# Optimization experiments

Measured on AMD Instinct MI355X. Metric: run time of the kernel, lower is better.

## Reference

```python
import jax, jax.numpy as jnp
import numpy as np

# graph/batch constants
B, N_PER, DEG, FEAT, K = 64, 1024, 16, 64, 10
N = B * N_PER            # 65536 total nodes
E = N * DEG              # 1048576 edges
HID = 2 * FEAT           # 128


def setup_inputs() -> dict:
    key = jax.random.key(0)
    ks = jax.random.split(key, 10)
    x = jax.random.normal(ks[0], (N, FEAT), jnp.float32)
    # intra-graph edges: local indices in [0, n) offset by graph id * n
    offs = (jnp.arange(B, dtype=jnp.int32) * N_PER)[:, None]
    edge_src = (jax.random.randint(ks[1], (B, N_PER * DEG), 0, N_PER, jnp.int32) + offs).reshape(-1)
    edge_dst = (jax.random.randint(ks[2], (B, N_PER * DEG), 0, N_PER, jnp.int32) + offs).reshape(-1)
    uniforms = jax.random.uniform(ks[3], (N, 3 * K), jnp.float32, 1e-6, 1.0 - 1e-6)

    def lin(k, i, o):
        s = 1.0 / np.sqrt(i)
        return jax.random.uniform(k, (i, o), jnp.float32, -s, s)

    return {
        "x": x, "edge_src": edge_src, "edge_dst": edge_dst, "uniforms": uniforms,
        "W0": lin(ks[4], FEAT, HID), "b0": jnp.zeros((HID,), jnp.float32),
        "W1": lin(ks[5], HID, HID), "b1": jnp.zeros((HID,), jnp.float32),
        "Wf": lin(ks[6], HID, HID), "bf": jnp.zeros((HID,), jnp.float32),
        "W2": lin(ks[7], 2 * HID, HID), "b2": jnp.zeros((HID,), jnp.float32),
        "W3": lin(ks[8], HID, 1), "b3": jnp.zeros((1,), jnp.float32),
    }


def _gcn_norm(src, dst):
    # GCNConv: add self-loops, symmetric deg^{-1/2} normalization
    loop = jnp.arange(N, dtype=src.dtype)
    s = jnp.concatenate([src, loop])
    d = jnp.concatenate([dst, loop])
    deg = jnp.zeros((N,), jnp.float32).at[d].add(1.0)
    dinv = jax.lax.rsqrt(deg)  # deg >= 1 because of self-loops
    return s, d, dinv[s] * dinv[d]


def _gcn(h, W, b, s, d, norm):
    h = h @ W                                                   # [N, out]
    agg = jnp.zeros((N, W.shape[1]), h.dtype).at[d].add(h[s] * norm[:, None])
    return agg + b


def reference(x, edge_src, edge_dst, uniforms, W0, b0, W1, b1, Wf, bf, W2, b2, W3, b3):
    s, d, norm = _gcn_norm(edge_src, edge_dst)
    # conv0 + global max pool + fc1 -> per-graph global info
    h0 = jax.nn.relu(_gcn(x, W0, b0, s, d, norm))               # [N, HID]
    glob = jnp.max(h0.reshape(B, N_PER, HID), axis=1) @ Wf + bf  # [B, HID]
    # two applications of the SAME conv1 (as in the source)
    h = jax.nn.relu(_gcn(h0, W1, b1, s, d, norm))
    h = jax.nn.relu(_gcn(h, W1, b1, s, d, norm))
    # ConcatenateLayer: [local, tiled global] per node (dropout is eval identity)
    h = jnp.concatenate([h, jnp.repeat(glob, N_PER, axis=0)], axis=-1)  # [N, 2*HID]
    h = jax.nn.relu(_gcn(h, W2, b2, s, d, norm))
    logits = _gcn(h, W3, b3, s, d, norm).reshape(B, N_PER)      # [B, n]
    # SampleConcrete (eval): per-graph top-k threshold mask
    th = jax.lax.top_k(logits, K)[0][:, -1]                     # kth-largest per graph
    mask = (logits >= th[:, None]).astype(jnp.float32)
    return mask.reshape(N, 1)
```

## Files before the change

kernel.cpp:

```cpp
#include <hip/hip_runtime.h>
#include <math.h>

#define NB    64
#define NPER  1024
#define NTOT  65536
#define ETOT  1048576
#define FEAT  64
#define HID   128
#define KSEL  10
#define MAXDEG 64


typedef __attribute__((ext_vector_type(8))) short bf16x8;
typedef __attribute__((ext_vector_type(4))) float f32x4;

#define ASLOT(a, q) (((a) << 2) + ((q) ^ (((a) >> 1) & 3)))
#define GSLOT(p, r) (((p) * 64 + ((r) ^ ((p) & 7))) * 8)

static __device__ __forceinline__ unsigned short f2bf(float x) {
    unsigned u = __float_as_uint(x);
    return (unsigned short)((u + 0x7FFFu + ((u >> 16) & 1u)) >> 16);
}
static __device__ __forceinline__ float bf2f(unsigned short s) {
    return __uint_as_float(((unsigned)s) << 16);
}

__global__ __launch_bounds__(256) void csr_k(const int* __restrict__ src,
                                             const int* __restrict__ dst,
                                             int* __restrict__ cnt,
                                             unsigned short* __restrict__ col16) {
    int e = blockIdx.x * 256 + threadIdx.x;
    if (e >= ETOT) return;
    int d = dst[e];
    int s = src[e];
    int pos = atomicAdd(&cnt[d], 1);
    col16[(size_t)pos * NTOT + d] = (unsigned short)(s & (NPER - 1));
}

__global__ __launch_bounds__(256) void pack_k(const float* __restrict__ W0,
                                              const float* __restrict__ W1,
                                              const float* __restrict__ W2,
                                              unsigned short* __restrict__ Wph,
                                              unsigned short* __restrict__ Wpl,
                                              float* __restrict__ part,
                                              int* __restrict__ cnt) {
    int t = blockIdx.x * 256 + threadIdx.x;
    for (int i = t; i < NTOT; i += 160 * 256) cnt[i] = 0;
    if (blockIdx.x == 0) {
        for (int i = threadIdx.x; i < NB * 128; i += 256) part[i] = 0.f;
    }
    if (t >= 320 * 128) return;
    int k = t >> 7;
    int c = t & 127;
    float v;
    size_t mb;
    int kk;
    if (k < 64)       { kk = k;       v = W0[kk * 128 + c]; mb = 0; }
    else if (k < 192) { kk = k - 64;  v = W1[kk * 128 + c]; mb = (size_t)64 * 128; }
    else              { kk = k - 192; v = W2[kk * 128 + c]; mb = (size_t)192 * 128; }
    unsigned short h  = f2bf(v);
    unsigned short lo = f2bf(v - bf2f(h));
    size_t d = mb + ((size_t)(kk >> 3) * 128 + c) * 8 + (kk & 7);
    Wph[d] = h;
    Wpl[d] = lo;
}

__global__ __launch_bounds__(1024) void agg_k(const float* __restrict__ Z,
                                              const float* __restrict__ x,
                                              const unsigned short* __restrict__ col16,
                                              const int* __restrict__ cnt,
                                              unsigned short* __restrict__ Ah,
                                              unsigned short* __restrict__ Al,
                                              int cshift,
                                              float* __restrict__ fvec,
                                              const float* __restrict__ Wf,
                                              const float* __restrict__ bfv,
                                              const float* __restrict__ W2g,
                                              float* __restrict__ gproj,
                                              const float* __restrict__ part) {
    __shared__ float4 sy4[4096];
    int t = threadIdx.x;

    if (Wf && (int)blockIdx.x >= (int)gridDim.x - NB) {
        float* sm = (float*)sy4;
        float* mp = sm;
        float* ps = sm + 128;
        float* gl = sm + 128 + 1024;
        int gg = blockIdx.x - (gridDim.x - NB);
        int o = t & 127, s8 = t >> 7;
        if (t < 128) mp[t] = part[(size_t)gg * 128 + t];
        __syncthreads();
        float p = 0.f;
#pragma unroll
        for (int q = 0; q < 16; ++q) { int k = s8 * 16 + q; p += mp[k] * Wf[(size_t)k * 128 + o]; }
        ps[t] = p;
        __syncthreads();
        if (t < 128) {
            float a = bfv[t];
#pragma unroll
            for (int q = 0; q < 8; ++q) a += ps[q * 128 + t];
            gl[t] = a;
        }
        __syncthreads();
        p = 0.f;
#pragma unroll
        for (int q = 0; q < 16; ++q) { int k = s8 * 16 + q; p += gl[k] * W2g[(size_t)(128 + k) * 128 + o]; }
        ps[t] = p;
        __syncthreads();
        if (t < 128) {
            float a = 0.f;
#pragma unroll
            for (int q = 0; q < 8; ++q) a += ps[q * 128 + t];
            gproj[(size_t)gg * 128 + t] = a;
        }
        return;
    }

    int g = blockIdx.x >> cshift;
    int c = blockIdx.x & ((1 << cshift) - 1);
    int gbase = g << 10;

    if (x) {
#pragma unroll
        for (int j = 0; j < 4; ++j) {
            int fl = j * 1024 + t;
            int v = fl >> 2, q = fl & 3;
            float dvv = rsqrtf((float)cnt[gbase + v] + 1.0f);
            float4 z = *(const float4*)&x[(size_t)(gbase + v) * FEAT + c * 16 + q * 4];
            z.x *= dvv; z.y *= dvv; z.z *= dvv; z.w *= dvv;
            sy4[ASLOT(v, q)] = z;
        }
    } else {
        const float4* Zg4 = (const float4*)(Z + ((size_t)c * NTOT + gbase) * 16);
#pragma unroll
        for (int j = 0; j < 4; ++j) {
            int fl = j * 1024 + t;
            int v = fl >> 2, q = fl & 3;
            sy4[ASLOT(v, q)] = Zg4[fl];
        }
    }
    __syncthreads();

    int f4 = t & 3;
    int vl = t >> 2;

#pragma unroll 1
    for (int pass = 0; pass < 4; ++pass) {
        int v = pass * 256 + vl;
        int gv = gbase + v;
        int n = cnt[gv];
        float dv = rsqrtf((float)n + 1.0f);
        const unsigned short* ip = col16 + gv;
        float4 acc = sy4[ASLOT(v, f4)];
        int i = 0;
        for (; i + 4 <= n; i += 4) {
            int a0 = ip[(size_t)(i + 0) * NTOT];
            int a1 = ip[(size_t)(i + 1) * NTOT];
            int a2 = ip[(size_t)(i + 2) * NTOT];
            int a3 = ip[(size_t)(i + 3) * NTOT];
            float4 y0 = sy4[ASLOT(a0, f4)];
            float4 y1 = sy4[ASLOT(a1, f4)];
            float4 y2 = sy4[ASLOT(a2, f4)];
            float4 y3 = sy4[ASLOT(a3, f4)];
            acc.x += (y0.x + y1.x) + (y2.x + y3.x);
            acc.y += (y0.y + y1.y) + (y2.y + y3.y);
            acc.z += (y0.z + y1.z) + (y2.z + y3.z);
            acc.w += (y0.w + y1.w) + (y2.w + y3.w);
        }
        for (; i < n; ++i) {
            int a = ip[(size_t)i * NTOT];
            float4 ya = sy4[ASLOT(a, f4)];
            acc.x += ya.x; acc.y += ya.y; acc.z += ya.z; acc.w += ya.w;
        }
        acc.x *= dv; acc.y *= dv; acc.z *= dv; acc.w *= dv;
        int krow = c * 16 + f4 * 4;
        size_t ba = ((size_t)(krow >> 3) * NTOT + gv) * 8 + (krow & 7);
        ushort4 h, lo;
        h.x = f2bf(acc.x); lo.x = f2bf(acc.x - bf2f(h.x));
        h.y = f2bf(acc.y); lo.y = f2bf(acc.y - bf2f(h.y));
        h.z = f2bf(acc.z); lo.z = f2bf(acc.z - bf2f(h.z));
        h.w = f2bf(acc.w); lo.w = f2bf(acc.w - bf2f(h.w));
        *(ushort4*)&Ah[ba] = h;
        *(ushort4*)&Al[ba] = lo;
    }

    if (fvec && c == 0) {
        __syncthreads();
        float* sdv = (float*)sy4;
        float dv = rsqrtf((float)cnt[gbase + t] + 1.0f);
        sdv[t] = dv;
        __syncthreads();
        int n = cnt[gbase + t];
        float acc = dv;
        const unsigned short* ip = col16 + gbase + t;
        for (int i = 0; i < n; ++i) acc += sdv[ip[(size_t)i * NTOT]];
        fvec[gbase + t] = dv * acc;
    }
}

__global__ __launch_bounds__(256, 4) void gemm_k(const unsigned short* __restrict__ Ah,
                                                 const unsigned short* __restrict__ Al,
                                                 const unsigned short* __restrict__ Wph,
                                                 const unsigned short* __restrict__ Wpl,
                                                 const float* __restrict__ bias,
                                                 float* __restrict__ outZ,
                                                 int K,
                                                 const float* __restrict__ fvec,
                                                 const float* __restrict__ gproj,
                                                 float* __restrict__ part,
                                                 const float* __restrict__ W3,
                                                 const int* __restrict__ cnt,
                                                 float* __restrict__ zout) {
    __shared__ __align__(16) unsigned short sAh[64 * 128];
    __shared__ __align__(16) unsigned short sAl[64 * 128];
    __shared__ float zred[4 * 64];

    int t = threadIdx.x;
    int row0 = blockIdx.x * 64;
    int w = t >> 6;
    int l = t & 63;
    int lr = l & 15;
    int hg = l >> 4;

    f32x4 acc[4][2];
#pragma unroll
    for (int m = 0; m < 4; ++m)
#pragma unroll
        for (int n = 0; n < 2; ++n) acc[m][n] = (f32x4){0.f, 0.f, 0.f, 0.f};

    int nu = (K >> 3) << 6 >> 8;
    for (int i = 0; i < nu; ++i) {
        int u = t + i * 256;
        int p = u >> 6, r = u & 63;
        size_t src = ((size_t)p * NTOT + row0 + r) * 8;
        *(uint4*)&sAh[GSLOT(p, r)] = *(const uint4*)&Ah[src];
        *(uint4*)&sAl[GSLOT(p, r)] = *(const uint4*)&Al[src];
    }
    __syncthreads();

    int nk = K >> 5;
#pragma unroll 1
    for (int s = 0; s < nk; ++s) {
        int pb = s * 4 + hg;
        bf16x8 ah[4], al[4], bh[2], bl[2];
#pragma unroll
        for (int m = 0; m < 4; ++m) {
            ah[m] = *(const bf16x8*)&sAh[GSLOT(pb, m * 16 + lr)];
            al[m] = *(const bf16x8*)&sAl[GSLOT(pb, m * 16 + lr)];
        }
#pragma unroll
        for (int n = 0; n < 2; ++n) {
            size_t wb = ((size_t)pb * 128 + w * 32 + n * 16 + lr) * 8;
            bh[n] = *(const bf16x8*)&Wph[wb];
            bl[n] = *(const bf16x8*)&Wpl[wb];
        }
#pragma unroll
        for (int m = 0; m < 4; ++m)
#pragma unroll
            for (int n = 0; n < 2; ++n) {
                acc[m][n] = __builtin_amdgcn_mfma_f32_16x16x32_bf16(ah[m], bh[n], acc[m][n], 0, 0, 0);
                acc[m][n] = __builtin_amdgcn_mfma_f32_16x16x32_bf16(al[m], bh[n], acc[m][n], 0, 0, 0);
                acc[m][n] = __builtin_amdgcn_mfma_f32_16x16x32_bf16(ah[m], bl[n], acc[m][n], 0, 0, 0);
            }
    }

    int g = row0 >> 10;
    int wc0 = w * 32;
    float bb[2], gp[2], w3c[2];
#pragma unroll
    for (int n = 0; n < 2; ++n) {
        int col = wc0 + n * 16 + lr;
        bb[n]  = bias[col];
        gp[n]  = fvec ? gproj[(size_t)g * 128 + col] : 0.f;
        w3c[n] = zout ? W3[col] : 0.f;
    }
    float fr[4][4];
    if (fvec) {
#pragma unroll
        for (int m = 0; m < 4; ++m)
#pragma unroll
            for (int r = 0; r < 4; ++r) fr[m][r] = fvec[row0 + m * 16 + hg * 4 + r];
    }
    float dvs[4][4];
    if (outZ) {
#pragma unroll
        for (int m = 0; m < 4; ++m)
#pragma unroll
            for (int r = 0; r < 4; ++r)
                dvs[m][r] = rsqrtf((float)cnt[row0 + m * 16 + hg * 4 + r] + 1.0f);
    }
    float zp[4][4];
#pragma unroll
    for (int m = 0; m < 4; ++m)
#pragma unroll
        for (int r = 0; r < 4; ++r) zp[m][r] = 0.f;
    float cmx[2] = {0.f, 0.f};

#pragma unroll
    for (int m = 0; m < 4; ++m)
#pragma unroll
        for (int n = 0; n < 2; ++n)
#pragma unroll
            for (int r = 0; r < 4; ++r) {
                float v = acc[m][n][r] + bb[n];
                if (fvec) v += fr[m][r] * gp[n];
                v = fmaxf(v, 0.f);
                if (part) cmx[n] = fmaxf(cmx[n], v);
                if (zout) zp[m][r] += v * w3c[n];
                if (outZ) {
                    int row = row0 + m * 16 + hg * 4 + r;
                    int cidx = w * 2 + n;
                    outZ[((size_t)cidx * NTOT + row) * 16 + lr] = v * dvs[m][r];
                }
            }

    if (part) {
#pragma unroll
        for (int n = 0; n < 2; ++n) {
            float v = cmx[n];
            v = fmaxf(v, __shfl_xor(v, 16));
            v = fmaxf(v, __shfl_xor(v, 32));
            if (hg == 0)
                atomicMax((int*)&part[(size_t)g * 128 + wc0 + n * 16 + lr],
                          __float_as_int(v));
        }
    }

    if (zout) {
#pragma unroll
        for (int m = 0; m < 4; ++m)
#pragma unroll
            for (int r = 0; r < 4; ++r) {
                float v = zp[m][r];
                v += __shfl_xor(v, 1);
                v += __shfl_xor(v, 2);
                v += __shfl_xor(v, 4);
                v += __shfl_xor(v, 8);
                zp[m][r] = v;
            }
        if (lr == 0) {
#pragma unroll
            for (int m = 0; m < 4; ++m)
#pragma unroll
                for (int r = 0; r < 4; ++r)
                    zred[w * 64 + m * 16 + hg * 4 + r] = zp[m][r];
        }
        __syncthreads();
        if (t < 64) {
            float sZ = zred[t] + zred[64 + t] + zred[128 + t] + zred[192 + t];
            zout[row0 + t] = sZ * rsqrtf((float)cnt[row0 + t] + 1.0f);
        }
    }
}

__global__ __launch_bounds__(1024) void smask_k(const float* __restrict__ z,
                                                const unsigned short* __restrict__ col16,
                                                const int* __restrict__ cnt,
                                                const float* __restrict__ b3,
                                                float* __restrict__ out) {
    __shared__ float sz[1024];
    __shared__ float sl[1024];
    __shared__ float slo[1024];
    __shared__ float rv[16];
    __shared__ int   ri[16];
    __shared__ float sth;
    int g = blockIdx.x, t = threadIdx.x;
    int wv = t >> 6, ln = t & 63;
    int base = g << 10;
    sz[t] = z[base + t];
    __syncthreads();
    float bb = b3[0];
    {
        int gv = base + t;
        int n = cnt[gv];
        float dv = rsqrtf((float)n + 1.0f);
        float acc = sz[t];
        const unsigned short* ip = col16 + gv;
        int j = 0;
        for (; j + 2 <= n; j += 2)
            acc += sz[ip[(size_t)j * NTOT]] + sz[ip[(size_t)(j + 1) * NTOT]];
        for (; j < n; ++j) acc += sz[ip[(size_t)j * NTOT]];
        float lg = acc * dv + bb;
        sl[t] = lg; slo[t] = lg;
    }
    __syncthreads();
    for (int pass = 0; pass < KSEL; ++pass) {
        float bv = sl[t];
        int bi = t;
#pragma unroll
        for (int off = 32; off; off >>= 1) {
            float ov = __shfl_xor(bv, off);
            int   oi = __shfl_xor(bi, off);
            if (ov > bv || (ov == bv && oi < bi)) { bv = ov; bi = oi; }
        }
        if (ln == 0) { rv[wv] = bv; ri[wv] = bi; }
        __syncthreads();
        if (t == 0) {
            float mv = rv[0]; int mi = ri[0];
#pragma unroll
            for (int q = 1; q < 16; ++q)
                if (rv[q] > mv || (rv[q] == mv && ri[q] < mi)) { mv = rv[q]; mi = ri[q]; }
            sth = mv; sl[mi] = -INFINITY;
        }
        __syncthreads();
    }
    float th = sth;
    out[base + t] = (slo[t] >= th) ? 1.f : 0.f;
}

extern "C" void kernel_launch(void* const* d_in, const int* in_sizes, int n_in,
                              void* d_out, int out_size, void* d_ws, size_t ws_size,
                              hipStream_t stream) {
    const float* x        = (const float*)d_in[0];
    const int*   edge_src = (const int*)d_in[1];
    const int*   edge_dst = (const int*)d_in[2];
    const float* W0 = (const float*)d_in[4];
    const float* b0 = (const float*)d_in[5];
    const float* W1 = (const float*)d_in[6];
    const float* b1 = (const float*)d_in[7];
    const float* Wf = (const float*)d_in[8];
    const float* bf = (const float*)d_in[9];
    const float* W2 = (const float*)d_in[10];
    const float* b2 = (const float*)d_in[11];
    const float* W3 = (const float*)d_in[12];
    const float* b3 = (const float*)d_in[13];
    float* out = (float*)d_out;

    char* w = (char*)d_ws;
    int*            cnt   = (int*)w;            w += (size_t)NTOT * 4;
    unsigned short* col16 = (unsigned short*)w; w += (size_t)NTOT * MAXDEG * 2;
    float*          fvec  = (float*)w;          w += (size_t)NTOT * 4;
    unsigned short* Ah    = (unsigned short*)w; w += (size_t)NTOT * 128 * 2;
    unsigned short* Al    = (unsigned short*)w; w += (size_t)NTOT * 128 * 2;
    float*          Q     = (float*)w;          w += (size_t)NTOT * 128 * 4;
    float*          part  = (float*)w;          w += (size_t)NB * 128 * 4;
    float*          gproj = (float*)w;          w += (size_t)NB * 128 * 4;
    float*          z     = (float*)w;          w += (size_t)NTOT * 4;
    unsigned short* Wph   = (unsigned short*)w; w += (size_t)320 * 128 * 2;
    unsigned short* Wpl   = (unsigned short*)w; w += (size_t)320 * 128 * 2;

    pack_k<<<160, 256, 0, stream>>>(W0, W1, W2, Wph, Wpl, part, cnt);
    csr_k<<<ETOT / 256, 256, 0, stream>>>(edge_src, edge_dst, cnt, col16);

    agg_k<<<NB * 4, 1024, 0, stream>>>(nullptr, x, col16, cnt, Ah, Al, 2, nullptr,
                                       nullptr, nullptr, nullptr, nullptr, nullptr);
    gemm_k<<<NTOT / 64, 256, 0, stream>>>(Ah, Al, Wph, Wpl, b0, Q, FEAT,
                                          nullptr, nullptr, part, nullptr, cnt, nullptr);

    agg_k<<<NB * 8 + NB, 1024, 0, stream>>>(Q, nullptr, col16, cnt, Ah, Al, 3, nullptr,
                                            Wf, bf, W2, gproj, part);
    gemm_k<<<NTOT / 64, 256, 0, stream>>>(Ah, Al, Wph + 64 * 128, Wpl + 64 * 128, b1, Q,
                                          HID, nullptr, nullptr, nullptr, nullptr, cnt,
                                          nullptr);
    agg_k<<<NB * 8, 1024, 0, stream>>>(Q, nullptr, col16, cnt, Ah, Al, 3, nullptr,
                                       nullptr, nullptr, nullptr, nullptr, nullptr);
    gemm_k<<<NTOT / 64, 256, 0, stream>>>(Ah, Al, Wph + 64 * 128, Wpl + 64 * 128, b1, Q,
                                          HID, nullptr, nullptr, nullptr, nullptr, cnt,
                                          nullptr);

    agg_k<<<NB * 8, 1024, 0, stream>>>(Q, nullptr, col16, cnt, Ah, Al, 3, fvec,
                                       nullptr, nullptr, nullptr, nullptr, nullptr);
    gemm_k<<<NTOT / 64, 256, 0, stream>>>(Ah, Al, Wph + 192 * 128, Wpl + 192 * 128, b2,
                                          nullptr, HID, fvec, gproj, nullptr, W3, cnt, z);

    smask_k<<<NB, 1024, 0, stream>>>(z, col16, cnt, b3, out);
}
```

Measured before the change: 317.2 us.

## Fuse neighbor aggregation into GEMM prologue for hidden GCN layers

For layers 1-3 the separate aggregation kernel is removed. The GEMM kernel now gathers neighbor rows straight from a row-major fp32 activation buffer, splits them into bf16 hi/lo in shared memory, and computes the fvec normalization inline. This avoids writing and re-reading the Ah/Al intermediates and saves three kernel launches. The global-feature projection moves into extra GEMM blocks. In exchange, each block now does a latency-bound gather with 8-byte per-lane loads, reading global memory instead of a shared-memory staged graph tile, and two Q buffers are used.

```diff
diff --git a/kernel.cpp b/kernel.cpp
--- a/kernel.cpp
+++ b/kernel.cpp
@@ -65,79 +65,25 @@
     Wpl[d] = lo;
 }
 
-__global__ __launch_bounds__(1024) void agg_k(const float* __restrict__ Z,
-                                              const float* __restrict__ x,
+__global__ __launch_bounds__(1024) void agg_k(const float* __restrict__ x,
                                               const unsigned short* __restrict__ col16,
                                               const int* __restrict__ cnt,
                                               unsigned short* __restrict__ Ah,
-                                              unsigned short* __restrict__ Al,
-                                              int cshift,
-                                              float* __restrict__ fvec,
-                                              const float* __restrict__ Wf,
-                                              const float* __restrict__ bfv,
-                                              const float* __restrict__ W2g,
-                                              float* __restrict__ gproj,
-                                              const float* __restrict__ part) {
+                                              unsigned short* __restrict__ Al) {
     __shared__ float4 sy4[4096];
     int t = threadIdx.x;
-
-    if (Wf && (int)blockIdx.x >= (int)gridDim.x - NB) {
-        float* sm = (float*)sy4;
-        float* mp = sm;
-        float* ps = sm + 128;
-        float* gl = sm + 128 + 1024;
-        int gg = blockIdx.x - (gridDim.x - NB);
-        int o = t & 127, s8 = t >> 7;
-        if (t < 128) mp[t] = part[(size_t)gg * 128 + t];
-        __syncthreads();
-        float p = 0.f;
-#pragma unroll
-        for (int q = 0; q < 16; ++q) { int k = s8 * 16 + q; p += mp[k] * Wf[(size_t)k * 128 + o]; }
-        ps[t] = p;
-        __syncthreads();
-        if (t < 128) {
-            float a = bfv[t];
-#pragma unroll
-            for (int q = 0; q < 8; ++q) a += ps[q * 128 + t];
-            gl[t] = a;
-        }
-        __syncthreads();
-        p = 0.f;
-#pragma unroll
-        for (int q = 0; q < 16; ++q) { int k = s8 * 16 + q; p += gl[k] * W2g[(size_t)(128 + k) * 128 + o]; }
-        ps[t] = p;
-        __syncthreads();
-        if (t < 128) {
-            float a = 0.f;
-#pragma unroll
-            for (int q = 0; q < 8; ++q) a += ps[q * 128 + t];
-            gproj[(size_t)gg * 128 + t] = a;
-        }
-        return;
-    }
-
-    int g = blockIdx.x >> cshift;
-    int c = blockIdx.x & ((1 << cshift) - 1);
+    int g = blockIdx.x >> 2;
+    int c = blockIdx.x & 3;
     int gbase = g << 10;
 
-    if (x) {
-#pragma unroll
-        for (int j = 0; j < 4; ++j) {
-            int fl = j * 1024 + t;
-            int v = fl >> 2, q = fl & 3;
-            float dvv = rsqrtf((float)cnt[gbase + v] + 1.0f);
-            float4 z = *(const float4*)&x[(size_t)(gbase + v) * FEAT + c * 16 + q * 4];
-            z.x *= dvv; z.y *= dvv; z.z *= dvv; z.w *= dvv;
-            sy4[ASLOT(v, q)] = z;
-        }
-    } else {
-        const float4* Zg4 = (const float4*)(Z + ((size_t)c * NTOT + gbase) * 16);
-#pragma unroll
-        for (int j = 0; j < 4; ++j) {
-            int fl = j * 1024 + t;
-            int v = fl >> 2, q = fl & 3;
-            sy4[ASLOT(v, q)] = Zg4[fl];
-        }
+#pragma unroll
+    for (int j = 0; j < 4; ++j) {
+        int fl = j * 1024 + t;
+        int v = fl >> 2, q = fl & 3;
+        float dvv = rsqrtf((float)cnt[gbase + v] + 1.0f);
+        float4 z = *(const float4*)&x[(size_t)(gbase + v) * FEAT + c * 16 + q * 4];
+        z.x *= dvv; z.y *= dvv; z.z *= dvv; z.w *= dvv;
+        sy4[ASLOT(v, q)] = z;
     }
     __syncthreads();
 
@@ -183,44 +129,63 @@
         *(ushort4*)&Ah[ba] = h;
         *(ushort4*)&Al[ba] = lo;
     }
-
-    if (fvec && c == 0) {
-        __syncthreads();
-        float* sdv = (float*)sy4;
-        float dv = rsqrtf((float)cnt[gbase + t] + 1.0f);
-        sdv[t] = dv;
-        __syncthreads();
-        int n = cnt[gbase + t];
-        float acc = dv;
-        const unsigned short* ip = col16 + gbase + t;
-        for (int i = 0; i < n; ++i) acc += sdv[ip[(size_t)i * NTOT]];
-        fvec[gbase + t] = dv * acc;
-    }
 }
 
 __global__ __launch_bounds__(256, 4) void gemm_k(const unsigned short* __restrict__ Ah,
                                                  const unsigned short* __restrict__ Al,
+                                                 const float* __restrict__ gsrc,
                                                  const unsigned short* __restrict__ Wph,
                                                  const unsigned short* __restrict__ Wpl,
                                                  const float* __restrict__ bias,
                                                  float* __restrict__ outZ,
                                                  int K,
-                                                 const float* __restrict__ fvec,
                                                  const float* __restrict__ gproj,
                                                  float* __restrict__ part,
                                                  const float* __restrict__ W3,
                                                  const int* __restrict__ cnt,
-                                                 float* __restrict__ zout) {
+                                                 const unsigned short* __restrict__ col16,
+                                                 float* __restrict__ zout,
+                                                 const float* __restrict__ partin,
+                                                 const float* __restrict__ Wf,
+                                                 const float* __restrict__ bfv,
+                                                 const float* __restrict__ W2g,
+                                                 float* __restrict__ globout) {
     __shared__ __align__(16) unsigned short sAh[64 * 128];
     __shared__ __align__(16) unsigned short sAl[64 * 128];
     __shared__ float zred[4 * 64];
+    __shared__ float fvl[64];
 
     int t = threadIdx.x;
+
+    if (globout && (int)blockIdx.x >= NTOT / 64) {
+        float* sm = (float*)sAh;
+        float* mp = sm;
+        float* ps = sm + 128;
+        float* gl = sm + 384;
+        int gg = blockIdx.x - NTOT / 64;
+        int o = t & 127, seg = t >> 7;
+        if (t < 128) mp[t] = partin[(size_t)gg * 128 + t];
+        __syncthreads();
+        float p = 0.f;
+        for (int q = 0; q < 64; ++q) { int k = seg * 64 + q; p += mp[k] * Wf[(size_t)k * 128 + o]; }
+        ps[t] = p;
+        __syncthreads();
+        if (t < 128) gl[t] = bfv[t] + ps[t] + ps[128 + t];
+        __syncthreads();
+        p = 0.f;
+        for (int q = 0; q < 64; ++q) { int k = seg * 64 + q; p += gl[k] * W2g[(size_t)(128 + k) * 128 + o]; }
+        ps[t] = p;
+        __syncthreads();
+        if (t < 128) globout[(size_t)gg * 128 + t] = ps[t] + ps[128 + t];
+        return;
+    }
+
     int row0 = blockIdx.x * 64;
     int w = t >> 6;
     int l = t & 63;
     int lr = l & 15;
     int hg = l >> 4;
+    bool use_f = (gproj != nullptr);
 
     f32x4 acc[4][2];
 #pragma unroll
@@ -228,13 +193,53 @@
 #pragma unroll
         for (int n = 0; n < 2; ++n) acc[m][n] = (f32x4){0.f, 0.f, 0.f, 0.f};
 
-    int nu = (K >> 3) << 6 >> 8;
-    for (int i = 0; i < nu; ++i) {
-        int u = t + i * 256;
-        int p = u >> 6, r = u & 63;
-        size_t src = ((size_t)p * NTOT + row0 + r) * 8;
-        *(uint4*)&sAh[GSLOT(p, r)] = *(const uint4*)&Ah[src];
-        *(uint4*)&sAl[GSLOT(p, r)] = *(const uint4*)&Al[src];
+    if (gsrc) {
+        int gb = row0 & ~(NPER - 1);
+        const float* qg = gsrc + (size_t)gb * 128;
+#pragma unroll 1
+        for (int rr = 0; rr < 16; ++rr) {
+            int row = row0 + w * 16 + rr;
+            int n = cnt[row];
+            const unsigned short* ip = col16 + row;
+            float2 a0 = *(const float2*)&gsrc[(size_t)row * 128 + l * 2];
+            float ax = a0.x, ay = a0.y;
+            float fs = 0.f;
+            int i = 0;
+            for (; i + 2 <= n; i += 2) {
+                int s0 = ip[(size_t)i * NTOT];
+                int s1 = ip[(size_t)(i + 1) * NTOT];
+                float2 y0 = *(const float2*)&qg[(size_t)s0 * 128 + l * 2];
+                float2 y1 = *(const float2*)&qg[(size_t)s1 * 128 + l * 2];
+                if (use_f)
+                    fs += rsqrtf((float)cnt[gb + s0] + 1.f) + rsqrtf((float)cnt[gb + s1] + 1.f);
+                ax += y0.x + y1.x;
+                ay += y0.y + y1.y;
+            }
+            if (i < n) {
+                int s0 = ip[(size_t)i * NTOT];
+                float2 y0 = *(const float2*)&qg[(size_t)s0 * 128 + l * 2];
+                if (use_f) fs += rsqrtf((float)cnt[gb + s0] + 1.f);
+                ax += y0.x;
+                ay += y0.y;
+            }
+            float dv = rsqrtf((float)n + 1.f);
+            ax *= dv; ay *= dv;
+            if (use_f && l == 0) fvl[w * 16 + rr] = dv * (dv + fs);
+            unsigned short hx = f2bf(ax), hy = f2bf(ay);
+            unsigned short lx = f2bf(ax - bf2f(hx)), ly = f2bf(ay - bf2f(hy));
+            int p = l >> 2, r = row - row0, off = (l & 3) * 2;
+            *(unsigned*)&sAh[GSLOT(p, r) + off] = (unsigned)hx | ((unsigned)hy << 16);
+            *(unsigned*)&sAl[GSLOT(p, r) + off] = (unsigned)lx | ((unsigned)ly << 16);
+        }
+    } else {
+        int nu = (K >> 3) << 6 >> 8;
+        for (int i = 0; i < nu; ++i) {
+            int u = t + i * 256;
+            int p = u >> 6, r = u & 63;
+            size_t src = ((size_t)p * NTOT + row0 + r) * 8;
+            *(uint4*)&sAh[GSLOT(p, r)] = *(const uint4*)&Ah[src];
+            *(uint4*)&sAl[GSLOT(p, r)] = *(const uint4*)&Al[src];
+        }
     }
     __syncthreads();
 
@@ -271,15 +276,15 @@
     for (int n = 0; n < 2; ++n) {
         int col = wc0 + n * 16 + lr;
         bb[n]  = bias[col];
-        gp[n]  = fvec ? gproj[(size_t)g * 128 + col] : 0.f;
+        gp[n]  = use_f ? gproj[(size_t)g * 128 + col] : 0.f;
         w3c[n] = zout ? W3[col] : 0.f;
     }
     float fr[4][4];
-    if (fvec) {
+    if (use_f) {
 #pragma unroll
         for (int m = 0; m < 4; ++m)
 #pragma unroll
-            for (int r = 0; r < 4; ++r) fr[m][r] = fvec[row0 + m * 16 + hg * 4 + r];
+            for (int r = 0; r < 4; ++r) fr[m][r] = fvl[m * 16 + hg * 4 + r];
     }
     float dvs[4][4];
     if (outZ) {
@@ -303,14 +308,13 @@
 #pragma unroll
             for (int r = 0; r < 4; ++r) {
                 float v = acc[m][n][r] + bb[n];
-                if (fvec) v += fr[m][r] * gp[n];
+                if (use_f) v += fr[m][r] * gp[n];
                 v = fmaxf(v, 0.f);
                 if (part) cmx[n] = fmaxf(cmx[n], v);
                 if (zout) zp[m][r] += v * w3c[n];
                 if (outZ) {
                     int row = row0 + m * 16 + hg * 4 + r;
-                    int cidx = w * 2 + n;
-                    outZ[((size_t)cidx * NTOT + row) * 16 + lr] = v * dvs[m][r];
+                    outZ[(size_t)row * 128 + wc0 + n * 16 + lr] = v * dvs[m][r];
                 }
             }
 
@@ -429,10 +433,10 @@
     char* w = (char*)d_ws;
     int*            cnt   = (int*)w;            w += (size_t)NTOT * 4;
     unsigned short* col16 = (unsigned short*)w; w += (size_t)NTOT * MAXDEG * 2;
-    float*          fvec  = (float*)w;          w += (size_t)NTOT * 4;
-    unsigned short* Ah    = (unsigned short*)w; w += (size_t)NTOT * 128 * 2;
-    unsigned short* Al    = (unsigned short*)w; w += (size_t)NTOT * 128 * 2;
+    unsigned short* Ah    = (unsigned short*)w; w += (size_t)NTOT * 64 * 2;
+    unsigned short* Al    = (unsigned short*)w; w += (size_t)NTOT * 64 * 2;
     float*          Q     = (float*)w;          w += (size_t)NTOT * 128 * 4;
+    float*          Qb    = (float*)w;          w += (size_t)NTOT * 128 * 4;
     float*          part  = (float*)w;          w += (size_t)NB * 128 * 4;
     float*          gproj = (float*)w;          w += (size_t)NB * 128 * 4;
     float*          z     = (float*)w;          w += (size_t)NTOT * 4;
@@ -442,26 +446,24 @@
     pack_k<<<160, 256, 0, stream>>>(W0, W1, W2, Wph, Wpl, part, cnt);
     csr_k<<<ETOT / 256, 256, 0, stream>>>(edge_src, edge_dst, cnt, col16);
 
-    agg_k<<<NB * 4, 1024, 0, stream>>>(nullptr, x, col16, cnt, Ah, Al, 2, nullptr,
-                                       nullptr, nullptr, nullptr, nullptr, nullptr);
-    gemm_k<<<NTOT / 64, 256, 0, stream>>>(Ah, Al, Wph, Wpl, b0, Q, FEAT,
-                                          nullptr, nullptr, part, nullptr, cnt, nullptr);
-
-    agg_k<<<NB * 8 + NB, 1024, 0, stream>>>(Q, nullptr, col16, cnt, Ah, Al, 3, nullptr,
-                                            Wf, bf, W2, gproj, part);
-    gemm_k<<<NTOT / 64, 256, 0, stream>>>(Ah, Al, Wph + 64 * 128, Wpl + 64 * 128, b1, Q,
-                                          HID, nullptr, nullptr, nullptr, nullptr, cnt,
-                                          nullptr);
-    agg_k<<<NB * 8, 1024, 0, stream>>>(Q, nullptr, col16, cnt, Ah, Al, 3, nullptr,
-                                       nullptr, nullptr, nullptr, nullptr, nullptr);
-    gemm_k<<<NTOT / 64, 256, 0, stream>>>(Ah, Al, Wph + 64 * 128, Wpl + 64 * 128, b1, Q,
-                                          HID, nullptr, nullptr, nullptr, nullptr, cnt,
-                                          nullptr);
-
-    agg_k<<<NB * 8, 1024, 0, stream>>>(Q, nullptr, col16, cnt, Ah, Al, 3, fvec,
-                                       nullptr, nullptr, nullptr, nullptr, nullptr);
-    gemm_k<<<NTOT / 64, 256, 0, stream>>>(Ah, Al, Wph + 192 * 128, Wpl + 192 * 128, b2,
-                                          nullptr, HID, fvec, gproj, nullptr, W3, cnt, z);
+    agg_k<<<NB * 4, 1024, 0, stream>>>(x, col16, cnt, Ah, Al);
+    gemm_k<<<NTOT / 64, 256, 0, stream>>>(Ah, Al, nullptr, Wph, Wpl, b0, Q, FEAT,
+                                          nullptr, part, nullptr, cnt, col16, nullptr,
+                                          nullptr, nullptr, nullptr, nullptr, nullptr);
+
+    gemm_k<<<NTOT / 64 + NB, 256, 0, stream>>>(nullptr, nullptr, Q,
+                                               Wph + 64 * 128, Wpl + 64 * 128, b1, Qb,
+                                               HID, nullptr, nullptr, nullptr, cnt,
+                                               col16, nullptr, part, Wf, bf, W2, gproj);
+    gemm_k<<<NTOT / 64, 256, 0, stream>>>(nullptr, nullptr, Qb,
+                                          Wph + 64 * 128, Wpl + 64 * 128, b1, Q, HID,
+                                          nullptr, nullptr, nullptr, cnt, col16, nullptr,
+                                          nullptr, nullptr, nullptr, nullptr, nullptr);
+
+    gemm_k<<<NTOT / 64, 256, 0, stream>>>(nullptr, nullptr, Q,
+                                          Wph + 192 * 128, Wpl + 192 * 128, b2, nullptr,
+                                          HID, gproj, nullptr, W3, cnt, col16, z,
+                                          nullptr, nullptr, nullptr, nullptr, nullptr);
 
     smask_k<<<NB, 1024, 0, stream>>>(z, col16, cnt, b3, out);
 }
```

Result: slower. 546.4 us (+72.3%).
